# Kernel optimization log

Measured on AMD Instinct MI355X. Metric: run time of the kernel, lower is better.

The kernel has to match this reference:

```python
import jax, jax.numpy as jnp
import numpy as np

NUM_LAYERS = 3


def setup_inputs() -> dict:
    key = jax.random.key(0)
    k1, k2 = jax.random.split(key)
    num_users, num_venues = 200000, 100000
    num_nodes = num_users + num_venues
    num_edges = 2_000_000
    embedding_dim = 64
    edge_index = jax.random.randint(k1, (2, num_edges), 0, num_nodes, dtype=jnp.int32)
    # nn.init.normal_(std=0.1)
    embedding = jax.random.normal(k2, (num_nodes, embedding_dim), dtype=jnp.float32) * 0.1
    return {"edge_index": edge_index, "embedding": embedding, "num_users": num_users}


def reference(edge_index, embedding, num_users):
    num_nodes, d = embedding.shape
    row, col = edge_index[0], edge_index[1]
    # symmetric-normalization coefficients (degree counts both endpoints, as in torch code)
    ones = jnp.ones(row.shape[0], dtype=embedding.dtype)
    deg = (jax.ops.segment_sum(ones, row, num_segments=num_nodes)
           + jax.ops.segment_sum(ones, col, num_segments=num_nodes))
    deg = jnp.maximum(deg, 1.0)
    deg_inv_sqrt = deg ** -0.5
    norm = deg_inv_sqrt[row] * deg_inv_sqrt[col]  # [E]

    emb = embedding
    layer_sum = embedding  # running sum of layer embeddings for the final mean
    for _ in range(NUM_LAYERS):
        msg = emb[col] * norm[:, None]                              # [E, d] gather-scale
        emb = jax.ops.segment_sum(msg, row, num_segments=num_nodes)  # [N, d] scatter-add
        layer_sum = layer_sum + emb
    final = layer_sum / (NUM_LAYERS + 1)
    return final[:num_users], final[num_users:]
```

## Files before the change

kernel.cpp:

```cpp
#include <hip/hip_runtime.h>

#define TPB 256

__global__ void k_build(const int* __restrict__ row, const int* __restrict__ col,
                        int* __restrict__ cntRow, int* __restrict__ cntCol,
                        int* __restrict__ slots, int E, int CAP) {
    int i = blockIdx.x * blockDim.x + threadIdx.x;
    if (i < E) {
        int r = row[i], c = col[i];
        int pos = atomicAdd(&cntRow[r], 1);
        if (pos < CAP) slots[(long)r * CAP + pos] = c;
        atomicAdd(&cntCol[c], 1);
    }
}

__global__ void k_dinv(const int* __restrict__ cntRow, const int* __restrict__ cntCol,
                       float* __restrict__ dinv, int N) {
    int i = blockIdx.x * blockDim.x + threadIdx.x;
    if (i < N) {
        int d = cntRow[i] + cntCol[i];
        float fd = (d < 1) ? 1.0f : (float)d;
        dinv[i] = 1.0f / sqrtf(fd);
    }
}

__global__ void k_gather(const float4* __restrict__ cur, float4* __restrict__ fnext,
                         const float4* __restrict__ base, float4* __restrict__ out,
                         const int* __restrict__ cnt, const int* __restrict__ slots,
                         const float* __restrict__ dinv, int N, int CAP, int mode) {
    long tid = (long)blockIdx.x * blockDim.x + threadIdx.x;
    int n = (int)(tid >> 4);
    if (n >= N) return;
    int q = (int)(tid & 15);

    int m = cnt[n];
    if (m > CAP) m = CAP;
    const int* sl = slots + (long)n * CAP;

    float4 acc = make_float4(0.f, 0.f, 0.f, 0.f);
    if (mode == 0) {
        for (int e = 0; e < m; ++e) {
            int c = sl[e];
            float s = dinv[c];
            float4 v = cur[((long)c << 4) + q];
            acc.x += v.x * s;
            acc.y += v.y * s;
            acc.z += v.z * s;
            acc.w += v.w * s;
        }
    } else {
        for (int e = 0; e < m; ++e) {
            int c = sl[e];
            float4 v = cur[((long)c << 4) + q];
            acc.x += v.x;
            acc.y += v.y;
            acc.z += v.z;
            acc.w += v.w;
        }
    }

    float di = dinv[n];
    long idx = ((long)n << 4) + q;
    float4 o = base[idx];
    o.x += acc.x * di; o.y += acc.y * di; o.z += acc.z * di; o.w += acc.w * di;
    if (mode == 2) {
        o.x *= 0.25f; o.y *= 0.25f; o.z *= 0.25f; o.w *= 0.25f;
    }
    out[idx] = o;
    if (mode != 2) {
        float d2 = di * di;
        acc.x *= d2; acc.y *= d2; acc.z *= d2; acc.w *= d2;
        fnext[idx] = acc;
    }
}

extern "C" void kernel_launch(void* const* d_in, const int* in_sizes, int n_in,
                              void* d_out, int out_size, void* d_ws, size_t ws_size,
                              hipStream_t stream) {
    const int*   edge_index = (const int*)d_in[0];
    const float* embedding  = (const float*)d_in[1];

    const int E = in_sizes[0] / 2;
    const int D = 64;
    const int N = in_sizes[1] / D;

    const int* row = edge_index;
    const int* col = edge_index + E;

    unsigned char* p = (unsigned char*)d_ws;
    auto alloc = [&](size_t bytes) -> void* {
        void* r = (void*)p;
        p += (bytes + 255) & ~(size_t)255;
        return r;
    };
    int*    cntRow = (int*)   alloc((size_t)N * sizeof(int));
    int*    cntCol = (int*)   alloc((size_t)N * sizeof(int));
    float*  dinv   = (float*) alloc((size_t)N * sizeof(float));
    float4* fA     = (float4*)alloc((size_t)N * D * sizeof(float));
    float4* fB     = (float4*)alloc((size_t)N * D * sizeof(float));

    size_t used = (size_t)(p - (unsigned char*)d_ws);
    long   capL = (ws_size > used) ? (long)((ws_size - used) / ((size_t)N * sizeof(int))) : 0;
    int    CAP  = (capL > 32) ? 32 : (int)capL;
    if (CAP < 4) CAP = 4;
    int* slots = (int*)alloc((size_t)N * CAP * sizeof(int));

    float4* out = (float4*)d_out;
    const float4* emb4 = (const float4*)embedding;

    hipMemsetAsync(cntRow, 0, (size_t)N * sizeof(int), stream);
    hipMemsetAsync(cntCol, 0, (size_t)N * sizeof(int), stream);
    k_build<<<(E + TPB - 1) / TPB, TPB, 0, stream>>>(row, col, cntRow, cntCol, slots, E, CAP);
    k_dinv<<<(N + TPB - 1) / TPB, TPB, 0, stream>>>(cntRow, cntCol, dinv, N);

    const long gthreads = (long)N * 16;
    const int gblocks = (int)((gthreads + TPB - 1) / TPB);

    k_gather<<<gblocks, TPB, 0, stream>>>(emb4, fA, emb4, out, cntRow, slots, dinv, N, CAP, 0);
    k_gather<<<gblocks, TPB, 0, stream>>>(fA, fB, out, out, cntRow, slots, dinv, N, CAP, 1);
    k_gather<<<gblocks, TPB, 0, stream>>>(fB, nullptr, out, out, cntRow, slots, dinv, N, CAP, 2);
}
```

Measured before the change: 670.2 us.

## Store intermediate gathered features in fp16 and prescale embeddings once

Adds a prescale kernel that multiplies each embedding row by its inverse-sqrt degree and stores it as fp16. All three propagation layers then gather fp16 rows, 128 bytes per node instead of 256, with 8 threads per node each handling 8 channels, and accumulate in fp32. This halves the random-gather traffic that dominates the layers, but adds an extra pass over the embedding and introduces fp16 rounding error in the propagated features.

```diff
diff --git a/kernel.cpp b/kernel.cpp
--- a/kernel.cpp
+++ b/kernel.cpp
@@ -1,6 +1,8 @@
 #include <hip/hip_runtime.h>
 
 #define TPB 256
+
+typedef _Float16 half_t;
 
 __global__ void k_build(const int* __restrict__ row, const int* __restrict__ col,
                         int* __restrict__ cntRow, int* __restrict__ cntCol,
@@ -24,53 +26,68 @@
     }
 }
 
-__global__ void k_gather(const float4* __restrict__ cur, float4* __restrict__ fnext,
+__global__ void k_prescale(const float4* __restrict__ emb, const float* __restrict__ dinv,
+                           float4* __restrict__ f, int N) {
+    long tid = (long)blockIdx.x * blockDim.x + threadIdx.x;
+    int n = (int)(tid >> 3);
+    if (n >= N) return;
+    int q = (int)(tid & 7);
+    float s = dinv[n];
+    long b = ((long)n << 4) + (q << 1);
+    float4 a0 = emb[b];
+    float4 a1 = emb[b + 1];
+    union { float4 f4; half_t h[8]; } u;
+    u.h[0] = (half_t)(a0.x * s); u.h[1] = (half_t)(a0.y * s);
+    u.h[2] = (half_t)(a0.z * s); u.h[3] = (half_t)(a0.w * s);
+    u.h[4] = (half_t)(a1.x * s); u.h[5] = (half_t)(a1.y * s);
+    u.h[6] = (half_t)(a1.z * s); u.h[7] = (half_t)(a1.w * s);
+    f[((long)n << 3) + q] = u.f4;
+}
+
+__global__ void k_gather(const float4* __restrict__ cur_h, float4* __restrict__ fnext,
                          const float4* __restrict__ base, float4* __restrict__ out,
                          const int* __restrict__ cnt, const int* __restrict__ slots,
                          const float* __restrict__ dinv, int N, int CAP, int mode) {
     long tid = (long)blockIdx.x * blockDim.x + threadIdx.x;
-    int n = (int)(tid >> 4);
+    int n = (int)(tid >> 3);
     if (n >= N) return;
-    int q = (int)(tid & 15);
+    int q = (int)(tid & 7);
 
     int m = cnt[n];
     if (m > CAP) m = CAP;
     const int* sl = slots + (long)n * CAP;
 
-    float4 acc = make_float4(0.f, 0.f, 0.f, 0.f);
-    if (mode == 0) {
-        for (int e = 0; e < m; ++e) {
-            int c = sl[e];
-            float s = dinv[c];
-            float4 v = cur[((long)c << 4) + q];
-            acc.x += v.x * s;
-            acc.y += v.y * s;
-            acc.z += v.z * s;
-            acc.w += v.w * s;
-        }
-    } else {
-        for (int e = 0; e < m; ++e) {
-            int c = sl[e];
-            float4 v = cur[((long)c << 4) + q];
-            acc.x += v.x;
-            acc.y += v.y;
-            acc.z += v.z;
-            acc.w += v.w;
-        }
+    float acc[8];
+#pragma unroll
+    for (int k = 0; k < 8; ++k) acc[k] = 0.0f;
+
+    for (int e = 0; e < m; ++e) {
+        int c = sl[e];
+        union { float4 f4; half_t h[8]; } u;
+        u.f4 = cur_h[((long)c << 3) + q];
+#pragma unroll
+        for (int k = 0; k < 8; ++k) acc[k] += (float)u.h[k];
     }
 
     float di = dinv[n];
-    long idx = ((long)n << 4) + q;
-    float4 o = base[idx];
-    o.x += acc.x * di; o.y += acc.y * di; o.z += acc.z * di; o.w += acc.w * di;
+    long b = ((long)n << 4) + (q << 1);
+    float4 o0 = base[b];
+    float4 o1 = base[b + 1];
+    o0.x += acc[0] * di; o0.y += acc[1] * di; o0.z += acc[2] * di; o0.w += acc[3] * di;
+    o1.x += acc[4] * di; o1.y += acc[5] * di; o1.z += acc[6] * di; o1.w += acc[7] * di;
     if (mode == 2) {
-        o.x *= 0.25f; o.y *= 0.25f; o.z *= 0.25f; o.w *= 0.25f;
+        o0.x *= 0.25f; o0.y *= 0.25f; o0.z *= 0.25f; o0.w *= 0.25f;
+        o1.x *= 0.25f; o1.y *= 0.25f; o1.z *= 0.25f; o1.w *= 0.25f;
     }
-    out[idx] = o;
+    out[b] = o0;
+    out[b + 1] = o1;
+
     if (mode != 2) {
         float d2 = di * di;
-        acc.x *= d2; acc.y *= d2; acc.z *= d2; acc.w *= d2;
-        fnext[idx] = acc;
+        union { float4 f4; half_t h[8]; } w;
+#pragma unroll
+        for (int k = 0; k < 8; ++k) w.h[k] = (half_t)(acc[k] * d2);
+        fnext[((long)n << 3) + q] = w.f4;
     }
 }
 
@@ -96,8 +113,9 @@
     int*    cntRow = (int*)   alloc((size_t)N * sizeof(int));
     int*    cntCol = (int*)   alloc((size_t)N * sizeof(int));
     float*  dinv   = (float*) alloc((size_t)N * sizeof(float));
-    float4* fA     = (float4*)alloc((size_t)N * D * sizeof(float));
-    float4* fB     = (float4*)alloc((size_t)N * D * sizeof(float));
+    float4* fA     = (float4*)alloc((size_t)N * D * sizeof(half_t));
+    float4* fB     = (float4*)alloc((size_t)N * D * sizeof(half_t));
+    float4* fC     = (float4*)alloc((size_t)N * D * sizeof(half_t));
 
     size_t used = (size_t)(p - (unsigned char*)d_ws);
     long   capL = (ws_size > used) ? (long)((ws_size - used) / ((size_t)N * sizeof(int))) : 0;
@@ -113,10 +131,11 @@
     k_build<<<(E + TPB - 1) / TPB, TPB, 0, stream>>>(row, col, cntRow, cntCol, slots, E, CAP);
     k_dinv<<<(N + TPB - 1) / TPB, TPB, 0, stream>>>(cntRow, cntCol, dinv, N);
 
-    const long gthreads = (long)N * 16;
-    const int gblocks = (int)((gthreads + TPB - 1) / TPB);
+    const long hthreads = (long)N * 8;
+    const int hblocks = (int)((hthreads + TPB - 1) / TPB);
+    k_prescale<<<hblocks, TPB, 0, stream>>>(emb4, dinv, fA, N);
 
-    k_gather<<<gblocks, TPB, 0, stream>>>(emb4, fA, emb4, out, cntRow, slots, dinv, N, CAP, 0);
-    k_gather<<<gblocks, TPB, 0, stream>>>(fA, fB, out, out, cntRow, slots, dinv, N, CAP, 1);
-    k_gather<<<gblocks, TPB, 0, stream>>>(fB, nullptr, out, out, cntRow, slots, dinv, N, CAP, 2);
+    k_gather<<<hblocks, TPB, 0, stream>>>(fA, fB, emb4, out, cntRow, slots, dinv, N, CAP, 1);
+    k_gather<<<hblocks, TPB, 0, stream>>>(fB, fC, out, out, cntRow, slots, dinv, N, CAP, 1);
+    k_gather<<<hblocks, TPB, 0, stream>>>(fC, nullptr, out, out, cntRow, slots, dinv, N, CAP, 2);
 }
```

Measured after the change: 550.4 us. 17.9% less time.
